# Optimization experiments

Hardware: AMD Instinct MI355X
Metric: run time of the kernel (lower is better)

## Reference

```python
import jax, jax.numpy as jnp
import numpy as np


def setup_inputs() -> dict:
    key = jax.random.key(0)
    ks = jax.random.split(key, 8)
    b, n, d = 4, 4096, 64
    scale = 1.0 / np.sqrt(d)
    return {
        "x": jax.random.normal(ks[0], (b, n, d), jnp.float32),
        "W1": jax.random.normal(ks[1], (d, d), jnp.float32) * scale,
        "b1": jax.random.normal(ks[2], (d,), jnp.float32) * 0.01,
        "W2": jax.random.normal(ks[3], (d, d), jnp.float32) * scale,
        "b2": jax.random.normal(ks[4], (d,), jnp.float32) * 0.01,
        "W3": jax.random.normal(ks[5], (d, d), jnp.float32) * scale,
        "b3": jax.random.normal(ks[6], (d,), jnp.float32) * 0.01,
        "temperature": jnp.array(4.0, jnp.float32),  # nn.Parameter init
        "k": 8,
    }


def reference(x, W1, b1, W2, b2, W3, b3, temperature, k):
    b, n, d = x.shape
    # MLP projection (torch Linear: y = x @ W.T + b)
    h = jax.nn.relu(x @ W1.T + b1)
    h = jax.nn.relu(h @ W2.T + b2)
    h = h @ W3.T + b3  # [b, n, d]

    tau = jnp.exp(jnp.clip(temperature, -5.0, 5.0))

    # pairwise squared euclidean distances [b, n, n]
    sq = jnp.sum(h * h, axis=-1)  # [b, n]
    dist = sq[:, :, None] + sq[:, None, :] - 2.0 * jnp.einsum("bnd,bmd->bnm", h, h)

    # argKmin over j (keops dim=1 reduction): k smallest scaled distances per row i
    _, idx = jax.lax.top_k(-(dist * tau), k)  # idx [b, n, k]

    idx_flat = idx.reshape(b, n * k)
    # gather neighbor features and recompute distances (as in the original)
    x1 = jnp.take_along_axis(h, idx_flat[:, :, None], axis=1)  # [b, n*k, d]
    x2 = jnp.repeat(h, k, axis=1)  # [b, n*k, d]
    dng = jnp.sum((x1 - x2) ** 2, axis=-1)  # [b, n*k]
    logprobs = (-dng * tau).reshape(b, n, k)

    rows = jnp.broadcast_to(jnp.arange(n)[None, :, None], (b, n, k)).reshape(b, n * k)
    edges = jnp.stack((idx_flat, rows), axis=-1)  # [b, n*k, 2]
    return edges, logprobs
```

## Files before the change

### kernel.cpp

```cpp
#include <hip/hip_runtime.h>
#include <math.h>

#define BB 4
#define NN 4096
#define DD 64
#define KK 8
#define CH 2

__device__ __forceinline__ float tau_of(const float* __restrict__ temp) {
  float tc = temp[0];
  tc = fminf(fmaxf(tc, -5.0f), 5.0f);
  return expf(tc);
}

__device__ __forceinline__ void ins_strict(float (&kk)[KK], int (&kj)[KK], float key, int j) {
  if (key < kk[KK - 1]) {
    kk[KK - 1] = key; kj[KK - 1] = j;
#pragma unroll
    for (int m = KK - 1; m > 0; --m) {
      if (kk[m] < kk[m - 1]) {
        float tk = kk[m]; kk[m] = kk[m - 1]; kk[m - 1] = tk;
        int tj = kj[m]; kj[m] = kj[m - 1]; kj[m - 1] = tj;
      }
    }
  }
}

__device__ __forceinline__ void ins_lex(float (&kk)[KK], int (&kj)[KK], float key, int j) {
  if (key < kk[KK - 1] || (key == kk[KK - 1] && j < kj[KK - 1])) {
    kk[KK - 1] = key; kj[KK - 1] = j;
#pragma unroll
    for (int m = KK - 1; m > 0; --m) {
      bool sw = (kk[m] < kk[m - 1]) || (kk[m] == kk[m - 1] && kj[m] < kj[m - 1]);
      if (sw) {
        float tk = kk[m]; kk[m] = kk[m - 1]; kk[m - 1] = tk;
        int tj = kj[m]; kj[m] = kj[m - 1]; kj[m - 1] = tj;
      }
    }
  }
}

__device__ __forceinline__ void mlp_layer(const float (*bin)[68], float (*bout)[68],
                                          float (*wT)[68], float* bias,
                                          const float* __restrict__ Wg,
                                          const float* __restrict__ bg,
                                          bool dorelu, int t) {
  const int rr = t >> 2;
  const int dc = (t & 3) << 4;
  {
    const float* wsrc = Wg + rr * DD + dc;
#pragma unroll
    for (int q = 0; q < 16; ++q) wT[dc + q][rr] = wsrc[q];
    if (t < DD) bias[t] = bg[t];
  }
  __syncthreads();
  const int tg = t & 15, og = t >> 4;
  float acc[4][4];
#pragma unroll
  for (int r = 0; r < 4; ++r)
#pragma unroll
    for (int c = 0; c < 4; ++c) acc[r][c] = 0.f;
#pragma unroll 4
  for (int i = 0; i < DD; ++i) {
    const float4 av = *reinterpret_cast<const float4*>(&bin[i][tg << 2]);
    const float4 wv = *reinterpret_cast<const float4*>(&wT[i][og << 2]);
    float aa[4] = {av.x, av.y, av.z, av.w};
    float ww[4] = {wv.x, wv.y, wv.z, wv.w};
#pragma unroll
    for (int r = 0; r < 4; ++r)
#pragma unroll
      for (int c = 0; c < 4; ++c) acc[r][c] += aa[r] * ww[c];
  }
#pragma unroll
  for (int r = 0; r < 4; ++r)
#pragma unroll
    for (int c = 0; c < 4; ++c) {
      float v = acc[r][c] + bias[(og << 2) + c];
      if (dorelu) v = fmaxf(v, 0.f);
      bout[(og << 2) + c][(tg << 2) + r] = v;
    }
  __syncthreads();
}

__global__ __launch_bounds__(256) void k_mlp(
    const float* __restrict__ x,
    const float* __restrict__ W1, const float* __restrict__ b1,
    const float* __restrict__ W2, const float* __restrict__ b2,
    const float* __restrict__ W3, const float* __restrict__ b3,
    float* __restrict__ h, float* __restrict__ sqo) {
  __shared__ float bufA[DD][68];
  __shared__ float bufB[DD][68];
  __shared__ float wT[DD][68];
  __shared__ float bias[DD];
  const int t = threadIdx.x;
  const size_t tok0 = (size_t)blockIdx.x * 64;
  const int rr = t >> 2;
  const int dc = (t & 3) << 4;
  {
    const float* src = x + (tok0 + rr) * DD + dc;
#pragma unroll
    for (int q = 0; q < 16; ++q) bufA[dc + q][rr] = src[q];
  }
  mlp_layer(bufA, bufB, wT, bias, W1, b1, true, t);
  mlp_layer(bufB, bufA, wT, bias, W2, b2, true, t);
  mlp_layer(bufA, bufB, wT, bias, W3, b3, false, t);
  {
    float s = 0.f;
    float* dst = h + (tok0 + rr) * DD + dc;
#pragma unroll
    for (int q = 0; q < 16; ++q) {
      float v = bufB[dc + q][rr];
      dst[q] = v;
      s += v * v;
    }
    s += __shfl_xor(s, 1);
    s += __shfl_xor(s, 2);
    if ((t & 3) == 0) sqo[tok0 + rr] = s;
  }
}

__global__ __launch_bounds__(256) void k_disttopk(
    const float* __restrict__ h, const float* __restrict__ sq,
    const float* __restrict__ temp,
    float* __restrict__ pk, int* __restrict__ pj) {
  __shared__ float hiT[DD][68];
  __shared__ float hjT[DD][68];
  __shared__ float sqi[64];
  __shared__ float sqj[64];
  __shared__ float distT[64][65];

  const int t = threadIdx.x;
  const int bx = blockIdx.x;
  const int b = bx >> 7;
  const int rt = (bx >> 1) & 63;
  const int ch = bx & 1;
  const int i0 = rt << 6;
  const float* hb = h + (size_t)b * NN * DD;
  const float* sqb = sq + b * NN;
  const float tau = tau_of(temp);

  const int rr = t >> 2;
  const int dc = (t & 3) << 4;
  {
    const float* src = hb + (size_t)(i0 + rr) * DD + dc;
#pragma unroll
    for (int q = 0; q < 16; ++q) hiT[dc + q][rr] = src[q];
    if (t < 64) sqi[t] = sqb[i0 + t];
  }

  float kk[KK]; int kj[KK];
#pragma unroll
  for (int m = 0; m < KK; ++m) { kk[m] = 3.0e38f; kj[m] = 0x7fffffff; }

  const int row = t & 63;
  const int qq = t >> 6;
  const int jbase = ch * (NN / CH);

  for (int jt = 0; jt < (NN / CH) / 64; ++jt) {
    const int j0 = jbase + (jt << 6);
    __syncthreads();
    {
      const float* src = hb + (size_t)(j0 + rr) * DD + dc;
#pragma unroll
      for (int q = 0; q < 16; ++q) hjT[dc + q][rr] = src[q];
      if (t < 64) sqj[t] = sqb[j0 + t];
    }
    __syncthreads();

    const int tg = t & 15, og = t >> 4;
    float acc[4][4];
#pragma unroll
    for (int r = 0; r < 4; ++r)
#pragma unroll
      for (int c = 0; c < 4; ++c) acc[r][c] = 0.f;
#pragma unroll 4
    for (int d = 0; d < DD; ++d) {
      const float4 av = *reinterpret_cast<const float4*>(&hiT[d][tg << 2]);
      const float4 bv = *reinterpret_cast<const float4*>(&hjT[d][og << 2]);
      float aa[4] = {av.x, av.y, av.z, av.w};
      float ww[4] = {bv.x, bv.y, bv.z, bv.w};
#pragma unroll
      for (int r = 0; r < 4; ++r)
#pragma unroll
        for (int c = 0; c < 4; ++c) acc[r][c] += aa[r] * ww[c];
    }
#pragma unroll
    for (int r = 0; r < 4; ++r)
#pragma unroll
      for (int c = 0; c < 4; ++c) {
        float s2 = __fadd_rn(sqi[(tg << 2) + r], sqj[(og << 2) + c]);
        float dd2 = __fsub_rn(s2, __fmul_rn(2.0f, acc[r][c]));
        distT[(tg << 2) + r][(og << 2) + c] = dd2;
      }
    __syncthreads();
#pragma unroll
    for (int s = 0; s < 16; ++s) {
      const int jj = (qq << 4) + s;
      const float key = __fmul_rn(distT[row][jj], tau);
      ins_strict(kk, kj, key, j0 + jj);
    }
  }
  __syncthreads();
  float* lk = &distT[0][0];
  int* lj = reinterpret_cast<int*>(&hjT[0][0]);
#pragma unroll
  for (int m = 0; m < KK; ++m) {
    lk[((row << 2) + qq) * KK + m] = kk[m];
    lj[((row << 2) + qq) * KK + m] = kj[m];
  }
  __syncthreads();
  if (t < 64) {
    float fk[KK]; int fj[KK];
#pragma unroll
    for (int m = 0; m < KK; ++m) { fk[m] = 3.0e38f; fj[m] = 0x7fffffff; }
    for (int q2 = 0; q2 < 4; ++q2) {
#pragma unroll
      for (int m = 0; m < KK; ++m) {
        float key = lk[((t << 2) + q2) * KK + m];
        int j = lj[((t << 2) + q2) * KK + m];
        ins_lex(fk, fj, key, j);
      }
    }
    const size_t base = ((size_t)(b * NN + i0 + t) * CH + ch) * KK;
#pragma unroll
    for (int m = 0; m < KK; ++m) { pk[base + m] = fk[m]; pj[base + m] = fj[m]; }
  }
}

__global__ __launch_bounds__(256) void k_final(
    const float* __restrict__ h, const float* __restrict__ pk,
    const int* __restrict__ pj, const float* __restrict__ temp,
    float* __restrict__ out) {
  const int gid = blockIdx.x * 256 + threadIdx.x;
  const int b = gid >> 12;
  const int i = gid & (NN - 1);
  const float tau = tau_of(temp);

  float fk[KK]; int fj[KK];
#pragma unroll
  for (int m = 0; m < KK; ++m) { fk[m] = 3.0e38f; fj[m] = 0x7fffffff; }
  const size_t base = (size_t)(b * NN + i) * CH * KK;
#pragma unroll
  for (int s = 0; s < CH * KK; ++s) {
    ins_lex(fk, fj, pk[base + s], pj[base + s]);
  }

  const float* hi = h + (size_t)(b * NN + i) * DD;
  float4 xi[16];
#pragma unroll
  for (int q = 0; q < 16; ++q) xi[q] = *reinterpret_cast<const float4*>(hi + (q << 2));

  float* oute = out;
  float* outl = out + (size_t)BB * NN * KK * 2;
#pragma unroll
  for (int m = 0; m < KK; ++m) {
    const int j = fj[m];
    const float* hj = h + (size_t)(b * NN + j) * DD;
    float dng = 0.f;
#pragma unroll
    for (int q = 0; q < 16; ++q) {
      const float4 vj = *reinterpret_cast<const float4*>(hj + (q << 2));
      float dx = xi[q].x - vj.x; dng += dx * dx;
      float dy = xi[q].y - vj.y; dng += dy * dy;
      float dz = xi[q].z - vj.z; dng += dz * dz;
      float dw = xi[q].w - vj.w; dng += dw * dw;
    }
    const size_t e = (size_t)(b * NN + i) * KK + m;
    oute[e * 2 + 0] = (float)j;
    oute[e * 2 + 1] = (float)i;
    outl[e] = -__fmul_rn(dng, tau);
  }
}

extern "C" void kernel_launch(void* const* d_in, const int* in_sizes, int n_in,
                              void* d_out, int out_size, void* d_ws, size_t ws_size,
                              hipStream_t stream) {
  const float* x  = (const float*)d_in[0];
  const float* W1 = (const float*)d_in[1];
  const float* b1 = (const float*)d_in[2];
  const float* W2 = (const float*)d_in[3];
  const float* b2 = (const float*)d_in[4];
  const float* W3 = (const float*)d_in[5];
  const float* b3 = (const float*)d_in[6];
  const float* temp = (const float*)d_in[7];
  (void)in_sizes; (void)n_in; (void)out_size; (void)ws_size;

  float* ws = (float*)d_ws;
  float* h  = ws;
  float* sq = h + (size_t)BB * NN * DD;
  float* pk = sq + (size_t)BB * NN;
  int*   pj = (int*)(pk + (size_t)BB * NN * CH * KK);
  float* out = (float*)d_out;

  k_mlp<<<BB * NN / 64, 256, 0, stream>>>(x, W1, b1, W2, b2, W3, b3, h, sq);
  k_disttopk<<<BB * (NN / 64) * CH, 256, 0, stream>>>(h, sq, temp, pk, pj);
  k_final<<<BB * NN / 256, 256, 0, stream>>>(h, pk, pj, temp, out);
}
```

Measured before the change: 276.5 us.

## Double-buffer j-tiles, keep per-thread top-k in registers, split columns into four chunks

The distance/top-k kernel now splits the column range into four chunks, giving twice as many blocks. It double-buffers the hj tile, prefetching the next tile into registers while the current one is computed. Each thread keeps four register-resident top-k lists, one per owned row, and inserts distances straight from the accumulators, which removes the shared-memory distance tile and one barrier per tile. A two-stage shared-memory merge then reduces the 16 partial lists per row. The cost is much higher register pressure under launch_bounds(256,3), more divergent insertion work per thread, and a longer final merge that also feeds k_final.

```diff
diff --git a/kernel.cpp b/kernel.cpp
--- a/kernel.cpp
+++ b/kernel.cpp
@@ -5,7 +5,8 @@
 #define NN 4096
 #define DD 64
 #define KK 8
-#define CH 2
+#define CH 4
+#define NT ((NN / CH) / 64)
 
 __device__ __forceinline__ float tau_of(const float* __restrict__ temp) {
   float tc = temp[0];
@@ -13,7 +14,7 @@
   return expf(tc);
 }
 
-__device__ __forceinline__ void ins_strict(float (&kk)[KK], int (&kj)[KK], float key, int j) {
+__device__ __forceinline__ void ins_strict(float* kk, int* kj, float key, int j) {
   if (key < kk[KK - 1]) {
     kk[KK - 1] = key; kj[KK - 1] = j;
 #pragma unroll
@@ -26,7 +27,7 @@
   }
 }
 
-__device__ __forceinline__ void ins_lex(float (&kk)[KK], int (&kj)[KK], float key, int j) {
+__device__ __forceinline__ void ins_lex(float* kk, int* kj, float key, int j) {
   if (key < kk[KK - 1] || (key == kk[KK - 1] && j < kj[KK - 1])) {
     kk[KK - 1] = key; kj[KK - 1] = j;
 #pragma unroll
@@ -38,6 +39,15 @@
       }
     }
   }
+}
+
+__device__ __forceinline__ void scatter16(float (*dst)[64], int dc, int col,
+                                          const float4& a, const float4& b,
+                                          const float4& c, const float4& d) {
+  dst[dc + 0][col] = a.x; dst[dc + 1][col] = a.y; dst[dc + 2][col] = a.z; dst[dc + 3][col] = a.w;
+  dst[dc + 4][col] = b.x; dst[dc + 5][col] = b.y; dst[dc + 6][col] = b.z; dst[dc + 7][col] = b.w;
+  dst[dc + 8][col] = c.x; dst[dc + 9][col] = c.y; dst[dc + 10][col] = c.z; dst[dc + 11][col] = c.w;
+  dst[dc + 12][col] = d.x; dst[dc + 13][col] = d.y; dst[dc + 14][col] = d.z; dst[dc + 15][col] = d.w;
 }
 
 __device__ __forceinline__ void mlp_layer(const float (*bin)[68], float (*bout)[68],
@@ -119,111 +129,170 @@
   }
 }
 
-__global__ __launch_bounds__(256) void k_disttopk(
+__global__ __launch_bounds__(256, 3) void k_disttopk(
     const float* __restrict__ h, const float* __restrict__ sq,
     const float* __restrict__ temp,
     float* __restrict__ pk, int* __restrict__ pj) {
-  __shared__ float hiT[DD][68];
-  __shared__ float hjT[DD][68];
-  __shared__ float sqi[64];
-  __shared__ float sqj[64];
-  __shared__ float distT[64][65];
+  __shared__ __align__(16) char smem[16384 + 32768 + 512];
+  float (*hiT)[64] = (float (*)[64])(smem);
+  float (*hjT0)[64] = (float (*)[64])(smem + 16384);
+  float (*hjT1)[64] = (float (*)[64])(smem + 16384 + 16384);
+  float* sqjS = (float*)(smem + 49152);
 
   const int t = threadIdx.x;
   const int bx = blockIdx.x;
-  const int b = bx >> 7;
-  const int rt = (bx >> 1) & 63;
-  const int ch = bx & 1;
+  const int b = bx >> 8;
+  const int rem = bx & 255;
+  const int rt = rem >> 2;
+  const int ch = rem & 3;
   const int i0 = rt << 6;
+  const int jbase = ch * (NN / CH);
   const float* hb = h + (size_t)b * NN * DD;
   const float* sqb = sq + b * NN;
   const float tau = tau_of(temp);
 
+  const int og = t & 15, tg = t >> 4;
+  const int r0 = tg << 2, c0 = og << 2;
   const int rr = t >> 2;
   const int dc = (t & 3) << 4;
+
   {
     const float* src = hb + (size_t)(i0 + rr) * DD + dc;
-#pragma unroll
-    for (int q = 0; q < 16; ++q) hiT[dc + q][rr] = src[q];
-    if (t < 64) sqi[t] = sqb[i0 + t];
-  }
-
-  float kk[KK]; int kj[KK];
-#pragma unroll
-  for (int m = 0; m < KK; ++m) { kk[m] = 3.0e38f; kj[m] = 0x7fffffff; }
-
-  const int row = t & 63;
-  const int qq = t >> 6;
-  const int jbase = ch * (NN / CH);
-
-  for (int jt = 0; jt < (NN / CH) / 64; ++jt) {
+    float4 f0 = *(const float4*)(src);
+    float4 f1 = *(const float4*)(src + 4);
+    float4 f2 = *(const float4*)(src + 8);
+    float4 f3 = *(const float4*)(src + 12);
+    scatter16(hiT, dc, rr, f0, f1, f2, f3);
+  }
+  {
+    const float* src = hb + (size_t)(jbase + rr) * DD + dc;
+    float4 f0 = *(const float4*)(src);
+    float4 f1 = *(const float4*)(src + 4);
+    float4 f2 = *(const float4*)(src + 8);
+    float4 f3 = *(const float4*)(src + 12);
+    scatter16(hjT0, dc, rr, f0, f1, f2, f3);
+    if (t < 64) sqjS[t] = sqb[jbase + t];
+  }
+  float sqi_r[4];
+#pragma unroll
+  for (int r = 0; r < 4; ++r) sqi_r[r] = sqb[i0 + r0 + r];
+
+  float kk[4][KK]; int kj[4][KK];
+#pragma unroll
+  for (int r = 0; r < 4; ++r)
+#pragma unroll
+    for (int m = 0; m < KK; ++m) { kk[r][m] = 3.0e38f; kj[r][m] = 0x7fffffff; }
+
+  __syncthreads();
+
+  for (int jt = 0; jt < NT; ++jt) {
+    const int p = jt & 1;
     const int j0 = jbase + (jt << 6);
+    float (*cur)[64] = p ? hjT1 : hjT0;
+    float (*nxt)[64] = p ? hjT0 : hjT1;
+    const float* sqc = sqjS + p * 64;
+
+    float4 pf0, pf1, pf2, pf3; float psq = 0.f;
+    const bool hasNext = (jt + 1 < NT);
+    if (hasNext) {
+      const float* src = hb + (size_t)(j0 + 64 + rr) * DD + dc;
+      pf0 = *(const float4*)(src);
+      pf1 = *(const float4*)(src + 4);
+      pf2 = *(const float4*)(src + 8);
+      pf3 = *(const float4*)(src + 12);
+      if (t < 64) psq = sqb[j0 + 64 + t];
+    }
+
+    float acc[4][4];
+#pragma unroll
+    for (int r = 0; r < 4; ++r)
+#pragma unroll
+      for (int c = 0; c < 4; ++c) acc[r][c] = 0.f;
+#pragma unroll 8
+    for (int d = 0; d < DD; ++d) {
+      const float4 av = *(const float4*)(&cur[d][0] - 0 + r0 + 0);
+      const float4 xv = *(const float4*)(&hiT[d][r0]);
+      const float4 bv = *(const float4*)(&cur[d][c0]);
+      (void)av;
+      float aa[4] = {xv.x, xv.y, xv.z, xv.w};
+      float wwv[4] = {bv.x, bv.y, bv.z, bv.w};
+#pragma unroll
+      for (int r = 0; r < 4; ++r)
+#pragma unroll
+        for (int c = 0; c < 4; ++c) acc[r][c] += aa[r] * wwv[c];
+    }
+    float sqjv[4];
+#pragma unroll
+    for (int c = 0; c < 4; ++c) sqjv[c] = sqc[c0 + c];
+#pragma unroll
+    for (int r = 0; r < 4; ++r) {
+#pragma unroll
+      for (int c = 0; c < 4; ++c) {
+        float dist = __fsub_rn(__fadd_rn(sqi_r[r], sqjv[c]), __fmul_rn(2.0f, acc[r][c]));
+        float key = __fmul_rn(dist, tau);
+        ins_strict(kk[r], kj[r], key, j0 + c0 + c);
+      }
+    }
+    if (hasNext) {
+      scatter16(nxt, dc, rr, pf0, pf1, pf2, pf3);
+      if (t < 64) sqjS[(p ^ 1) * 64 + t] = psq;
+    }
     __syncthreads();
-    {
-      const float* src = hb + (size_t)(j0 + rr) * DD + dc;
-#pragma unroll
-      for (int q = 0; q < 16; ++q) hjT[dc + q][rr] = src[q];
-      if (t < 64) sqj[t] = sqb[j0 + t];
-    }
+  }
+
+  float* dK = (float*)(smem + 16384);
+  int*   dJ = (int*)(smem + 16384 + 16384);
+  float* oK = (float*)(smem);
+  int*   oJ = (int*)(smem + 4096);
+
+  for (int pass = 0; pass < 2; ++pass) {
     __syncthreads();
-
-    const int tg = t & 15, og = t >> 4;
-    float acc[4][4];
-#pragma unroll
-    for (int r = 0; r < 4; ++r)
-#pragma unroll
-      for (int c = 0; c < 4; ++c) acc[r][c] = 0.f;
-#pragma unroll 4
-    for (int d = 0; d < DD; ++d) {
-      const float4 av = *reinterpret_cast<const float4*>(&hiT[d][tg << 2]);
-      const float4 bv = *reinterpret_cast<const float4*>(&hjT[d][og << 2]);
-      float aa[4] = {av.x, av.y, av.z, av.w};
-      float ww[4] = {bv.x, bv.y, bv.z, bv.w};
-#pragma unroll
-      for (int r = 0; r < 4; ++r)
-#pragma unroll
-        for (int c = 0; c < 4; ++c) acc[r][c] += aa[r] * ww[c];
-    }
-#pragma unroll
-    for (int r = 0; r < 4; ++r)
-#pragma unroll
-      for (int c = 0; c < 4; ++c) {
-        float s2 = __fadd_rn(sqi[(tg << 2) + r], sqj[(og << 2) + c]);
-        float dd2 = __fsub_rn(s2, __fmul_rn(2.0f, acc[r][c]));
-        distT[(tg << 2) + r][(og << 2) + c] = dd2;
-      }
+#pragma unroll
+    for (int rr2 = 0; rr2 < 2; ++rr2) {
+      const int r = 2 * pass + rr2;
+      const int lr = tg * 2 + rr2;
+#pragma unroll
+      for (int m = 0; m < KK; ++m) {
+        dK[(lr * 16 + og) * KK + m] = kk[r][m];
+        dJ[(lr * 16 + og) * KK + m] = kj[r][m];
+      }
+    }
     __syncthreads();
-#pragma unroll
-    for (int s = 0; s < 16; ++s) {
-      const int jj = (qq << 4) + s;
-      const float key = __fmul_rn(distT[row][jj], tau);
-      ins_strict(kk, kj, key, j0 + jj);
-    }
-  }
-  __syncthreads();
-  float* lk = &distT[0][0];
-  int* lj = reinterpret_cast<int*>(&hjT[0][0]);
-#pragma unroll
-  for (int m = 0; m < KK; ++m) {
-    lk[((row << 2) + qq) * KK + m] = kk[m];
-    lj[((row << 2) + qq) * KK + m] = kj[m];
-  }
-  __syncthreads();
-  if (t < 64) {
-    float fk[KK]; int fj[KK];
-#pragma unroll
-    for (int m = 0; m < KK; ++m) { fk[m] = 3.0e38f; fj[m] = 0x7fffffff; }
-    for (int q2 = 0; q2 < 4; ++q2) {
+    if (t < 128) {
+      const int lr = t >> 2, q = t & 3;
+      float fk[KK]; int fj[KK];
+#pragma unroll
+      for (int m = 0; m < KK; ++m) { fk[m] = 3.0e38f; fj[m] = 0x7fffffff; }
+      for (int o2 = 0; o2 < 4; ++o2) {
+#pragma unroll
+        for (int m = 0; m < KK; ++m) {
+          ins_lex(fk, fj, dK[(lr * 16 + 4 * q + o2) * KK + m],
+                          dJ[(lr * 16 + 4 * q + o2) * KK + m]);
+        }
+      }
 #pragma unroll
       for (int m = 0; m < KK; ++m) {
-        float key = lk[((t << 2) + q2) * KK + m];
-        int j = lj[((t << 2) + q2) * KK + m];
-        ins_lex(fk, fj, key, j);
-      }
-    }
-    const size_t base = ((size_t)(b * NN + i0 + t) * CH + ch) * KK;
-#pragma unroll
-    for (int m = 0; m < KK; ++m) { pk[base + m] = fk[m]; pj[base + m] = fj[m]; }
+        oK[(lr * 4 + q) * KK + m] = fk[m];
+        oJ[(lr * 4 + q) * KK + m] = fj[m];
+      }
+    }
+    __syncthreads();
+    if (t < 32) {
+      const int lr = t;
+      const int row = 4 * (lr >> 1) + 2 * pass + (lr & 1);
+      float fk[KK]; int fj[KK];
+#pragma unroll
+      for (int m = 0; m < KK; ++m) { fk[m] = 3.0e38f; fj[m] = 0x7fffffff; }
+      for (int q2 = 0; q2 < 4; ++q2) {
+#pragma unroll
+        for (int m = 0; m < KK; ++m) {
+          ins_lex(fk, fj, oK[(lr * 4 + q2) * KK + m], oJ[(lr * 4 + q2) * KK + m]);
+        }
+      }
+      const size_t base = ((size_t)(b * NN + i0 + row) * CH + ch) * KK;
+#pragma unroll
+      for (int m = 0; m < KK; ++m) { pk[base + m] = fk[m]; pj[base + m] = fj[m]; }
+    }
   }
 }
 
@@ -240,7 +309,6 @@
 #pragma unroll
   for (int m = 0; m < KK; ++m) { fk[m] = 3.0e38f; fj[m] = 0x7fffffff; }
   const size_t base = (size_t)(b * NN + i) * CH * KK;
-#pragma unroll
   for (int s = 0; s < CH * KK; ++s) {
     ins_lex(fk, fj, pk[base + s], pj[base + s]);
   }
```

After: 520.5 us. 1.88x slower.

## Fuse top-k into GEMM registers with warp thresholds, med3 insertion, 3-way split

Applied to the files above, without the earlier changes.

The distance kernel now computes a 4x8 register tile per thread over 128-column j tiles and inserts keys straight from registers into per-row top-8 lists. This drops the shared-memory distance staging and its extra barrier. Each row's candidates are pre-filtered by a threshold that takes the minimum of the 8th-best value across the 16 threads sharing the row. Insertion now uses a branchless fmed3-based network, j is split into 3 chunks for more blocks, and a two-level shared-memory merge combines the 16 partial lists per row. The costs are higher register pressure (4 top-k lists per thread) and an uneven chunk split of 11/11/10 tiles.

```diff
diff --git a/kernel.cpp b/kernel.cpp
--- a/kernel.cpp
+++ b/kernel.cpp
@@ -5,7 +5,16 @@
 #define NN 4096
 #define DD 64
 #define KK 8
-#define CH 2
+#define NCH 3
+
+#if defined(__has_builtin)
+#if __has_builtin(__builtin_amdgcn_fmed3f)
+#define FMED3(a, x, b) __builtin_amdgcn_fmed3f((x), (a), (b))
+#endif
+#endif
+#ifndef FMED3
+#define FMED3(a, x, b) fminf(fmaxf((a), (x)), (b))
+#endif
 
 __device__ __forceinline__ float tau_of(const float* __restrict__ temp) {
   float tc = temp[0];
@@ -13,31 +22,32 @@
   return expf(tc);
 }
 
-__device__ __forceinline__ void ins_strict(float (&kk)[KK], int (&kj)[KK], float key, int j) {
-  if (key < kk[KK - 1]) {
-    kk[KK - 1] = key; kj[KK - 1] = j;
-#pragma unroll
-    for (int m = KK - 1; m > 0; --m) {
-      if (kk[m] < kk[m - 1]) {
-        float tk = kk[m]; kk[m] = kk[m - 1]; kk[m - 1] = tk;
-        int tj = kj[m]; kj[m] = kj[m - 1]; kj[m - 1] = tj;
-      }
-    }
-  }
-}
-
-__device__ __forceinline__ void ins_lex(float (&kk)[KK], int (&kj)[KK], float key, int j) {
-  if (key < kk[KK - 1] || (key == kk[KK - 1] && j < kj[KK - 1])) {
-    kk[KK - 1] = key; kj[KK - 1] = j;
-#pragma unroll
-    for (int m = KK - 1; m > 0; --m) {
-      bool sw = (kk[m] < kk[m - 1]) || (kk[m] == kk[m - 1] && kj[m] < kj[m - 1]);
-      if (sw) {
-        float tk = kk[m]; kk[m] = kk[m - 1]; kk[m - 1] = tk;
-        int tj = kj[m]; kj[m] = kj[m - 1]; kj[m - 1] = tj;
-      }
-    }
-  }
+__device__ __forceinline__ void ins_med3(float (&kk)[KK], int (&kj)[KK], float key, int j) {
+  const bool l0 = key < kk[0], l1 = key < kk[1], l2 = key < kk[2], l3 = key < kk[3];
+  const bool l4 = key < kk[4], l5 = key < kk[5], l6 = key < kk[6], l7 = key < kk[7];
+  kj[7] = l6 ? kj[6] : (l7 ? j : kj[7]);  kk[7] = FMED3(kk[6], key, kk[7]);
+  kj[6] = l5 ? kj[5] : (l6 ? j : kj[6]);  kk[6] = FMED3(kk[5], key, kk[6]);
+  kj[5] = l4 ? kj[4] : (l5 ? j : kj[5]);  kk[5] = FMED3(kk[4], key, kk[5]);
+  kj[4] = l3 ? kj[3] : (l4 ? j : kj[4]);  kk[4] = FMED3(kk[3], key, kk[4]);
+  kj[3] = l2 ? kj[2] : (l3 ? j : kj[3]);  kk[3] = FMED3(kk[2], key, kk[3]);
+  kj[2] = l1 ? kj[1] : (l2 ? j : kj[2]);  kk[2] = FMED3(kk[1], key, kk[2]);
+  kj[1] = l0 ? kj[0] : (l1 ? j : kj[1]);  kk[1] = FMED3(kk[0], key, kk[1]);
+  kj[0] = l0 ? j : kj[0];                 kk[0] = fminf(kk[0], key);
+}
+
+__device__ __forceinline__ void ins_lexm(float (&kk)[KK], int (&kj)[KK], float key, int j) {
+  bool l[KK];
+#pragma unroll
+  for (int m = 0; m < KK; ++m)
+    l[m] = (key < kk[m]) || (key == kk[m] && j < kj[m]);
+  kj[7] = l[6] ? kj[6] : (l[7] ? j : kj[7]);  kk[7] = FMED3(kk[6], key, kk[7]);
+  kj[6] = l[5] ? kj[5] : (l[6] ? j : kj[6]);  kk[6] = FMED3(kk[5], key, kk[6]);
+  kj[5] = l[4] ? kj[4] : (l[5] ? j : kj[5]);  kk[5] = FMED3(kk[4], key, kk[5]);
+  kj[4] = l[3] ? kj[3] : (l[4] ? j : kj[4]);  kk[4] = FMED3(kk[3], key, kk[4]);
+  kj[3] = l[2] ? kj[2] : (l[3] ? j : kj[3]);  kk[3] = FMED3(kk[2], key, kk[3]);
+  kj[2] = l[1] ? kj[1] : (l[2] ? j : kj[2]);  kk[2] = FMED3(kk[1], key, kk[2]);
+  kj[1] = l[0] ? kj[0] : (l[1] ? j : kj[1]);  kk[1] = FMED3(kk[0], key, kk[1]);
+  kj[0] = l[0] ? j : kj[0];                   kk[0] = fminf(kk[0], key);
 }
 
 __device__ __forceinline__ void mlp_layer(const float (*bin)[68], float (*bout)[68],
@@ -119,112 +129,197 @@
   }
 }
 
-__global__ __launch_bounds__(256) void k_disttopk(
+__device__ __forceinline__ void merge_pass(
+    char* smem, int t, int roff, int b, int i0, int ch,
+    float (&kkx)[KK], int (&kjx)[KK],
+    float* __restrict__ pk, int* __restrict__ pj) {
+  float* dK = (float*)(smem);
+  int* dJ = (int*)(smem + 8192);
+  float* oK = (float*)(smem + 16384);
+  int* oJ = (int*)(smem + 16384 + 2048);
+  const int rg = t >> 4, cg = t & 15;
+  __syncthreads();
+#pragma unroll
+  for (int m = 0; m < KK; ++m) {
+    dK[(rg * 16 + cg) * KK + m] = kkx[m];
+    dJ[(rg * 16 + cg) * KK + m] = kjx[m];
+  }
+  __syncthreads();
+  if (t < 64) {
+    const int row16 = t >> 2, q = t & 3;
+    float fk[KK]; int fj[KK];
+#pragma unroll
+    for (int m = 0; m < KK; ++m) { fk[m] = 3.0e38f; fj[m] = 0x7fffffff; }
+#pragma unroll
+    for (int o = 0; o < 4; ++o)
+#pragma unroll
+      for (int m = 0; m < KK; ++m)
+        ins_lexm(fk, fj, dK[(row16 * 16 + q * 4 + o) * KK + m],
+                         dJ[(row16 * 16 + q * 4 + o) * KK + m]);
+#pragma unroll
+    for (int m = 0; m < KK; ++m) {
+      oK[(row16 * 4 + q) * KK + m] = fk[m];
+      oJ[(row16 * 4 + q) * KK + m] = fj[m];
+    }
+  }
+  __syncthreads();
+  if (t < 16) {
+    float gk[KK]; int gj[KK];
+#pragma unroll
+    for (int m = 0; m < KK; ++m) { gk[m] = 3.0e38f; gj[m] = 0x7fffffff; }
+#pragma unroll
+    for (int q = 0; q < 4; ++q)
+#pragma unroll
+      for (int m = 0; m < KK; ++m)
+        ins_lexm(gk, gj, oK[(t * 4 + q) * KK + m], oJ[(t * 4 + q) * KK + m]);
+    const size_t base = ((size_t)(b * NN + i0 + (t << 2) + roff) * NCH + ch) * KK;
+#pragma unroll
+    for (int m = 0; m < KK; ++m) { pk[base + m] = gk[m]; pj[base + m] = gj[m]; }
+  }
+}
+
+__global__ __launch_bounds__(256, 3) void k_disttopk(
     const float* __restrict__ h, const float* __restrict__ sq,
     const float* __restrict__ temp,
     float* __restrict__ pk, int* __restrict__ pj) {
-  __shared__ float hiT[DD][68];
-  __shared__ float hjT[DD][68];
-  __shared__ float sqi[64];
-  __shared__ float sqj[64];
-  __shared__ float distT[64][65];
+  __shared__ __align__(16) char smem[16384 + 32768 + 512];
+  float (*hiT)[64] = (float (*)[64])(smem);
+  float* hjT = (float*)(smem + 16384);
+  float* sqjS = (float*)(smem + 49152);
 
   const int t = threadIdx.x;
   const int bx = blockIdx.x;
-  const int b = bx >> 7;
-  const int rt = (bx >> 1) & 63;
-  const int ch = bx & 1;
+  const int b = bx / 192;
+  const int rem = bx % 192;
+  const int rt = rem / 3;
+  const int ch = rem % 3;
   const int i0 = rt << 6;
+  const int dt0 = (ch == 0) ? 0 : ((ch == 1) ? 11 : 22);
+  const int dt1 = (ch == 0) ? 11 : ((ch == 1) ? 22 : 32);
   const float* hb = h + (size_t)b * NN * DD;
   const float* sqb = sq + b * NN;
   const float tau = tau_of(temp);
 
-  const int rr = t >> 2;
-  const int dc = (t & 3) << 4;
+  const int rg = t >> 4, cg = t & 15;
+  const int r0 = rg << 2;
+  const int c0 = cg << 3;
+  const int pb0 = (((2 * cg) ^ cg) << 2);
+  const int pb1 = (((2 * cg + 1) ^ cg) << 2);
+
   {
-    const float* src = hb + (size_t)(i0 + rr) * DD + dc;
-#pragma unroll
-    for (int q = 0; q < 16; ++q) hiT[dc + q][rr] = src[q];
-    if (t < 64) sqi[t] = sqb[i0 + t];
-  }
-
-  float kk[KK]; int kj[KK];
-#pragma unroll
-  for (int m = 0; m < KK; ++m) { kk[m] = 3.0e38f; kj[m] = 0x7fffffff; }
-
-  const int row = t & 63;
-  const int qq = t >> 6;
-  const int jbase = ch * (NN / CH);
-
-  for (int jt = 0; jt < (NN / CH) / 64; ++jt) {
-    const int j0 = jbase + (jt << 6);
+    const int tok = t & 63, dch = t >> 6;
+    const float* src = hb + (size_t)(i0 + tok) * DD + (dch << 4);
+    const float4 f0 = *(const float4*)(src);
+    const float4 f1 = *(const float4*)(src + 4);
+    const float4 f2 = *(const float4*)(src + 8);
+    const float4 f3 = *(const float4*)(src + 12);
+    const int d0 = dch << 4;
+    hiT[d0 + 0][tok] = f0.x; hiT[d0 + 1][tok] = f0.y; hiT[d0 + 2][tok] = f0.z; hiT[d0 + 3][tok] = f0.w;
+    hiT[d0 + 4][tok] = f1.x; hiT[d0 + 5][tok] = f1.y; hiT[d0 + 6][tok] = f1.z; hiT[d0 + 7][tok] = f1.w;
+    hiT[d0 + 8][tok] = f2.x; hiT[d0 + 9][tok] = f2.y; hiT[d0 + 10][tok] = f2.z; hiT[d0 + 11][tok] = f2.w;
+    hiT[d0 + 12][tok] = f3.x; hiT[d0 + 13][tok] = f3.y; hiT[d0 + 14][tok] = f3.z; hiT[d0 + 15][tok] = f3.w;
+  }
+  float sqi0 = sqb[i0 + r0 + 0];
+  float sqi1 = sqb[i0 + r0 + 1];
+  float sqi2 = sqb[i0 + r0 + 2];
+  float sqi3 = sqb[i0 + r0 + 3];
+
+  float kk0[KK], kk1[KK], kk2[KK], kk3[KK];
+  int kj0[KK], kj1[KK], kj2[KK], kj3[KK];
+#pragma unroll
+  for (int m = 0; m < KK; ++m) {
+    kk0[m] = 3.0e38f; kj0[m] = 0x7fffffff;
+    kk1[m] = 3.0e38f; kj1[m] = 0x7fffffff;
+    kk2[m] = 3.0e38f; kj2[m] = 0x7fffffff;
+    kk3[m] = 3.0e38f; kj3[m] = 0x7fffffff;
+  }
+
+  const int tokJ = t & 127;
+  const int dchJ = t >> 7;
+  const int cbJ = tokJ >> 2;
+  const int pcol = (((cbJ ^ (cbJ >> 1)) << 2) | (tokJ & 3));
+
+  for (int dt = dt0; dt < dt1; ++dt) {
+    const int j0 = dt << 7;
     __syncthreads();
     {
-      const float* src = hb + (size_t)(j0 + rr) * DD + dc;
-#pragma unroll
-      for (int q = 0; q < 16; ++q) hjT[dc + q][rr] = src[q];
-      if (t < 64) sqj[t] = sqb[j0 + t];
+      const float* src = hb + (size_t)(j0 + tokJ) * DD + (dchJ << 5);
+      float4 f[8];
+#pragma unroll
+      for (int q = 0; q < 8; ++q) f[q] = *(const float4*)(src + (q << 2));
+      const int dbase = dchJ << 5;
+#pragma unroll
+      for (int q = 0; q < 8; ++q) {
+        hjT[(size_t)(dbase + (q << 2) + 0) * 128 + pcol] = f[q].x;
+        hjT[(size_t)(dbase + (q << 2) + 1) * 128 + pcol] = f[q].y;
+        hjT[(size_t)(dbase + (q << 2) + 2) * 128 + pcol] = f[q].z;
+        hjT[(size_t)(dbase + (q << 2) + 3) * 128 + pcol] = f[q].w;
+      }
+      if (t < 128) sqjS[t] = sqb[j0 + t];
     }
     __syncthreads();
 
-    const int tg = t & 15, og = t >> 4;
-    float acc[4][4];
+    float th0 = kk0[7], th1 = kk1[7], th2 = kk2[7], th3 = kk3[7];
+#pragma unroll
+    for (int msk = 1; msk <= 8; msk <<= 1) {
+      th0 = fminf(th0, __shfl_xor(th0, msk));
+      th1 = fminf(th1, __shfl_xor(th1, msk));
+      th2 = fminf(th2, __shfl_xor(th2, msk));
+      th3 = fminf(th3, __shfl_xor(th3, msk));
+    }
+
+    float acc[4][8];
 #pragma unroll
     for (int r = 0; r < 4; ++r)
 #pragma unroll
-      for (int c = 0; c < 4; ++c) acc[r][c] = 0.f;
+      for (int c = 0; c < 8; ++c) acc[r][c] = 0.f;
+    {
+      const float* pA = &hiT[0][r0];
+      const float* pB0 = hjT + pb0;
+      const float* pB1 = hjT + pb1;
 #pragma unroll 4
-    for (int d = 0; d < DD; ++d) {
-      const float4 av = *reinterpret_cast<const float4*>(&hiT[d][tg << 2]);
-      const float4 bv = *reinterpret_cast<const float4*>(&hjT[d][og << 2]);
-      float aa[4] = {av.x, av.y, av.z, av.w};
-      float ww[4] = {bv.x, bv.y, bv.z, bv.w};
-#pragma unroll
-      for (int r = 0; r < 4; ++r)
-#pragma unroll
-        for (int c = 0; c < 4; ++c) acc[r][c] += aa[r] * ww[c];
-    }
-#pragma unroll
-    for (int r = 0; r < 4; ++r)
-#pragma unroll
-      for (int c = 0; c < 4; ++c) {
-        float s2 = __fadd_rn(sqi[(tg << 2) + r], sqj[(og << 2) + c]);
-        float dd2 = __fsub_rn(s2, __fmul_rn(2.0f, acc[r][c]));
-        distT[(tg << 2) + r][(og << 2) + c] = dd2;
-      }
-    __syncthreads();
-#pragma unroll
-    for (int s = 0; s < 16; ++s) {
-      const int jj = (qq << 4) + s;
-      const float key = __fmul_rn(distT[row][jj], tau);
-      ins_strict(kk, kj, key, j0 + jj);
-    }
-  }
-  __syncthreads();
-  float* lk = &distT[0][0];
-  int* lj = reinterpret_cast<int*>(&hjT[0][0]);
-#pragma unroll
-  for (int m = 0; m < KK; ++m) {
-    lk[((row << 2) + qq) * KK + m] = kk[m];
-    lj[((row << 2) + qq) * KK + m] = kj[m];
-  }
-  __syncthreads();
-  if (t < 64) {
-    float fk[KK]; int fj[KK];
-#pragma unroll
-    for (int m = 0; m < KK; ++m) { fk[m] = 3.0e38f; fj[m] = 0x7fffffff; }
-    for (int q2 = 0; q2 < 4; ++q2) {
-#pragma unroll
-      for (int m = 0; m < KK; ++m) {
-        float key = lk[((t << 2) + q2) * KK + m];
-        int j = lj[((t << 2) + q2) * KK + m];
-        ins_lex(fk, fj, key, j);
-      }
-    }
-    const size_t base = ((size_t)(b * NN + i0 + t) * CH + ch) * KK;
-#pragma unroll
-    for (int m = 0; m < KK; ++m) { pk[base + m] = fk[m]; pj[base + m] = fj[m]; }
-  }
+      for (int d = 0; d < DD; ++d) {
+        const float4 av = *(const float4*)(pA);
+        const float4 b0v = *(const float4*)(pB0);
+        const float4 b1v = *(const float4*)(pB1);
+        pA += 64; pB0 += 128; pB1 += 128;
+        const float aa[4] = {av.x, av.y, av.z, av.w};
+        const float bb[8] = {b0v.x, b0v.y, b0v.z, b0v.w, b1v.x, b1v.y, b1v.z, b1v.w};
+#pragma unroll
+        for (int r = 0; r < 4; ++r)
+#pragma unroll
+          for (int c = 0; c < 8; ++c) acc[r][c] += aa[r] * bb[c];
+      }
+    }
+    const float4 sj0v = *(const float4*)(&sqjS[c0]);
+    const float4 sj1v = *(const float4*)(&sqjS[c0 + 4]);
+    const float sj[8] = {sj0v.x, sj0v.y, sj0v.z, sj0v.w, sj1v.x, sj1v.y, sj1v.z, sj1v.w};
+#pragma unroll
+    for (int c = 0; c < 8; ++c) {
+      const int j = j0 + c0 + c;
+      {
+        float key = __fmul_rn(__fsub_rn(__fadd_rn(sqi0, sj[c]), __fmul_rn(2.0f, acc[0][c])), tau);
+        if (key < th0) ins_med3(kk0, kj0, key, j);
+      }
+      {
+        float key = __fmul_rn(__fsub_rn(__fadd_rn(sqi1, sj[c]), __fmul_rn(2.0f, acc[1][c])), tau);
+        if (key < th1) ins_med3(kk1, kj1, key, j);
+      }
+      {
+        float key = __fmul_rn(__fsub_rn(__fadd_rn(sqi2, sj[c]), __fmul_rn(2.0f, acc[2][c])), tau);
+        if (key < th2) ins_med3(kk2, kj2, key, j);
+      }
+      {
+        float key = __fmul_rn(__fsub_rn(__fadd_rn(sqi3, sj[c]), __fmul_rn(2.0f, acc[3][c])), tau);
+        if (key < th3) ins_med3(kk3, kj3, key, j);
+      }
+    }
+  }
+
+  merge_pass(smem, t, 0, b, i0, ch, kk0, kj0, pk, pj);
+  merge_pass(smem, t, 1, b, i0, ch, kk1, kj1, pk, pj);
+  merge_pass(smem, t, 2, b, i0, ch, kk2, kj2, pk, pj);
+  merge_pass(smem, t, 3, b, i0, ch, kk3, kj3, pk, pj);
 }
 
 __global__ __launch_bounds__(256) void k_final(
@@ -239,10 +334,10 @@
   float fk[KK]; int fj[KK];
 #pragma unroll
   for (int m = 0; m < KK; ++m) { fk[m] = 3.0e38f; fj[m] = 0x7fffffff; }
-  const size_t base = (size_t)(b * NN + i) * CH * KK;
-#pragma unroll
-  for (int s = 0; s < CH * KK; ++s) {
-    ins_lex(fk, fj, pk[base + s], pj[base + s]);
+  const size_t base = (size_t)(b * NN + i) * NCH * KK;
+#pragma unroll
+  for (int s = 0; s < NCH * KK; ++s) {
+    ins_lexm(fk, fj, pk[base + s], pj[base + s]);
   }
 
   const float* hi = h + (size_t)(b * NN + i) * DD;
@@ -289,10 +384,10 @@
   float* h  = ws;
   float* sq = h + (size_t)BB * NN * DD;
   float* pk = sq + (size_t)BB * NN;
-  int*   pj = (int*)(pk + (size_t)BB * NN * CH * KK);
+  int*   pj = (int*)(pk + (size_t)BB * NN * NCH * KK);
   float* out = (float*)d_out;
 
   k_mlp<<<BB * NN / 64, 256, 0, stream>>>(x, W1, b1, W2, b2, W3, b3, h, sq);
-  k_disttopk<<<BB * (NN / 64) * CH, 256, 0, stream>>>(h, sq, temp, pk, pj);
+  k_disttopk<<<BB * 64 * NCH, 256, 0, stream>>>(h, sq, temp, pk, pj);
   k_final<<<BB * NN / 256, 256, 0, stream>>>(h, pk, pj, temp, out);
 }
```

Result: slower. 507.1 us (+83.4%).
